# Kernel tuning notes

Hardware: AMD Instinct MI355X
Metric: run time of the kernel (lower is better)

Reference implementation:

```python
import jax, jax.numpy as jnp
import numpy as np

N = 4096
IN_F = 512
OUT_F = 64
HEADS = 4
ALPHA = 0.2  # leaky relu slope
NEG_INF = -9e15


def setup_inputs() -> dict:
    key = jax.random.key(0)
    k1, k2, k3, k4 = jax.random.split(key, 4)
    x = jax.random.normal(k1, (N, IN_F), dtype=jnp.float32)
    adj = jax.random.randint(k2, (N, N), 0, 2, dtype=jnp.int32)
    # xavier-uniform-like init for params
    limW = float(np.sqrt(6.0 / (IN_F + OUT_F * HEADS)))
    W = jax.random.uniform(k3, (IN_F, OUT_F * HEADS), dtype=jnp.float32, minval=-limW, maxval=limW)
    lima = float(np.sqrt(6.0 / (2 * OUT_F + 1)))
    a = jax.random.uniform(k4, (2 * OUT_F, 1), dtype=jnp.float32, minval=-lima, maxval=lima)
    return {"x": x, "adj": adj, "W": W, "a": a}


def reference(x, adj, W, a):
    # h: [N, H, F]
    h = (x @ W).reshape(N, HEADS, OUT_F)
    a_src = a[:OUT_F, 0]   # [F]
    a_dst = a[OUT_F:, 0]   # [F]
    s = jnp.einsum("nhf,f->nh", h, a_src)  # source-node score [N, H]
    t = jnp.einsum("nhf,f->nh", h, a_dst)  # dest-node score   [N, H]
    # e[i, j, k] = leaky_relu(s[i,k] + t[j,k]) -> [N, N, H]
    e = jax.nn.leaky_relu(s[:, None, :] + t[None, :, :], negative_slope=ALPHA)
    mask = (adj > 0)[:, :, None]  # [N, N, 1]
    e = jnp.where(mask, e, NEG_INF)
    attn = jax.nn.softmax(e, axis=1)  # softmax over neighbors j
    # weighted aggregation per head: [N, H, F]
    h_prime = jnp.einsum("ijh,jhf->ihf", attn, h)
    return h_prime.reshape(N, HEADS * OUT_F)
```

## Files before the change

kernel.cpp:

```cpp
#include <hip/hip_runtime.h>
#include <hip/hip_bf16.h>


#define NN 4096
#define KF 512
#define NF 256

typedef __attribute__((ext_vector_type(8))) short bf16x8;
typedef __attribute__((ext_vector_type(4))) short s16x4;
typedef __attribute__((ext_vector_type(4))) float f32x4;

union AB8 { bf16x8 v; short2 h[4]; short s[8]; int4 i4; };
union ST4 { s16x4 v; short2 h[2]; };
union I64 { long v; int i[2]; };

__device__ __forceinline__ short f2bf(float f) {
    union { float f; unsigned u; } v; v.f = f;
    unsigned r = v.u + 0x7fffu + ((v.u >> 16) & 1u);
    return (short)(r >> 16);
}
__device__ __forceinline__ short2 pkbf(float a, float b) {
    __hip_bfloat162 t = __float22bfloat162_rn(make_float2(a, b));
    union { __hip_bfloat162 v; short2 s; } u; u.v = t;
    return u.s;
}
__device__ __forceinline__ int pkfp8x4(float a, float b, float c, float d) {
    int p = __builtin_amdgcn_cvt_pk_fp8_f32(a, b, 0, false);
    p     = __builtin_amdgcn_cvt_pk_fp8_f32(c, d, p, true);
    return p;
}

__global__ __launch_bounds__(256) void xpack(const float* __restrict__ x,
                                             short* __restrict__ xF) {
    const int lane = threadIdx.x & 63, wv = threadIdx.x >> 6;
    const int i = blockIdx.x * 4 + wv;
    const float4* xp = (const float4*)(x + (size_t)i * KF + lane * 8);
    float4 xa = xp[0], xb = xp[1];
    ST4 o0, o1;
    o0.h[0] = pkbf(xa.x, xa.y); o0.h[1] = pkbf(xa.z, xa.w);
    o1.h[0] = pkbf(xb.x, xb.y); o1.h[1] = pkbf(xb.z, xb.w);
    const int kblk = lane >> 2, qk = lane & 3;
    const int jgrp = i >> 4, r = i & 15;
    short* dst = xF + ((size_t)(kblk * 256 + jgrp) * 64 + qk * 16 + r) * 8;
    *(s16x4*)dst = o0.v;
    *(s16x4*)(dst + 4) = o1.v;
}

__global__ __launch_bounds__(256) void wpack(const float* __restrict__ W,
                                             short* __restrict__ WtF) {
    int tid = blockIdx.x * 256 + threadIdx.x;
    int l = tid & 63, nt = (tid >> 6) & 3, hd = (tid >> 8) & 3, kblk = tid >> 10;
    int q = l >> 4, r = l & 15;
    int col = hd * 64 + nt * 16 + r;
    int k0 = kblk * 32 + q * 8;
    AB8 o;
    #pragma unroll
    for (int e = 0; e < 8; e++) o.s[e] = f2bf(W[(k0 + e) * NF + col]);
    *(bf16x8*)(WtF + (size_t)tid * 8) = o.v;
}

__global__ __launch_bounds__(256) void adjpack(const int* __restrict__ adj,
                                               unsigned* __restrict__ pT) {
    int gw   = (blockIdx.x * 256 + threadIdx.x) >> 6;
    int lane = threadIdx.x & 63;
    int i = gw >> 4, seg = gw & 15;
    const int* ap = adj + (size_t)i * NN + seg * 256 + lane;
    unsigned long long b0 = __ballot(ap[0]   != 0);
    unsigned long long b1 = __ballot(ap[64]  != 0);
    unsigned long long b2 = __ballot(ap[128] != 0);
    unsigned long long b3 = __ballot(ap[192] != 0);
    if (lane == 0) {
        *(uint4*)(pT + ((size_t)(seg * 2    ) * NN + i) * 4) =
            make_uint4((unsigned)b0, (unsigned)(b0 >> 32), (unsigned)b1, (unsigned)(b1 >> 32));
        *(uint4*)(pT + ((size_t)(seg * 2 + 1) * NN + i) * 4) =
            make_uint4((unsigned)b2, (unsigned)(b2 >> 32), (unsigned)b3, (unsigned)(b3 >> 32));
    }
}

__global__ __launch_bounds__(256) void gemmfuse(const short* __restrict__ xF,
                                                const short* __restrict__ WtF,
                                                const float* __restrict__ a,
                                                unsigned char* __restrict__ VtF8,
                                                float* __restrict__ ipk,
                                                float2* __restrict__ jpk) {
    const int lane = threadIdx.x & 63, wv = threadIdx.x >> 6;
    const int q = lane >> 4, r = lane & 15;
    const int jb32 = blockIdx.x >> 1, ch = blockIdx.x & 1;
    const int rg = wv >> 1, hd = ch * 2 + (wv & 1);
    const int jgrp = jb32 * 2 + rg;

    const short* ap = xF  + ((size_t)jgrp * 64 + lane) * 8;
    const short* wp = WtF + ((size_t)(hd * 4) * 64 + lane) * 8;

    f32x4 acc[4] = {};
    #pragma unroll
    for (int kblk = 0; kblk < 16; kblk++) {
        bf16x8 av = *(const bf16x8*)(ap + (size_t)kblk * 256 * 512);
        const short* w = wp + (size_t)kblk * 16 * 512;
        #pragma unroll
        for (int nt = 0; nt < 4; nt++) {
            bf16x8 bv = *(const bf16x8*)(w + nt * 512);
            acc[nt] = __builtin_amdgcn_mfma_f32_16x16x32_bf16(av, bv, acc[nt], 0, 0, 0);
        }
    }

    const int base = rg * 16 + q * 4;
    const int qa = base >> 3, e0 = base & 7;
    #pragma unroll
    for (int nt = 0; nt < 4; nt++) {
        size_t slot = (size_t)(((jb32 * 4 + hd) * 4 + nt) * 64 + qa * 16 + r);
        *(int*)(VtF8 + slot * 8 + e0) = pkfp8x4(acc[nt][0], acc[nt][1], acc[nt][2], acc[nt][3]);
    }

    float as[4], at[4];
    #pragma unroll
    for (int nt = 0; nt < 4; nt++) { as[nt] = a[nt * 16 + r]; at[nt] = a[64 + nt * 16 + r]; }
    f32x4 sp = {}, tp = {};
    #pragma unroll
    for (int nt = 0; nt < 4; nt++)
        #pragma unroll
        for (int reg = 0; reg < 4; reg++) {
            sp[reg] += acc[nt][reg] * as[nt];
            tp[reg] += acc[nt][reg] * at[nt];
        }
    #pragma unroll
    for (int d = 1; d < 16; d <<= 1)
        #pragma unroll
        for (int reg = 0; reg < 4; reg++) {
            sp[reg] += __shfl_xor(sp[reg], d, 64);
            tp[reg] += __shfl_xor(tp[reg], d, 64);
        }
    if (r == 0) {
        #pragma unroll
        for (int reg = 0; reg < 4; reg++) {
            int j = jb32 * 32 + rg * 16 + q * 4 + reg;
            ipk[hd * NN + j] = __expf(-0.8f * sp[reg]);
            jpk[hd * NN + j] = make_float2(__expf(tp[reg]), __expf(0.2f * tp[reg]));
        }
    }
}

struct PF { float4 ja, jb, jc, jd; long v0, v1, v2, v3; };

__global__ __launch_bounds__(1024) __attribute__((amdgpu_waves_per_eu(1, 4)))
void gat_attn(const uint4* __restrict__ pT4, const float* __restrict__ ipk,
              const float* __restrict__ jpkf, const unsigned char* __restrict__ VtF8,
              float* __restrict__ out) {
    const int tid = threadIdx.x, lane = tid & 63, wv = tid >> 6;
    const int hd = wv & 3, jq = wv >> 2;
    const int q = lane >> 4, r = lane & 15;
    const int i0 = blockIdx.x * 16, i = i0 + r;
    const float ci = ipk[hd * NN + i];
    const int qs = q * 8;
    const float* jpf = jpkf + (size_t)hd * NN * 2;

    f32x4 acc[5] = {};
    const long ones = 0x3838383838383838L;

    auto load_pf = [&](PF& p, int it) {
        const float4* jp = (const float4*)(jpf + 2 * ((jq << 10) + (it << 5) + qs));
        p.ja = jp[0]; p.jb = jp[1]; p.jc = jp[2]; p.jd = jp[3];
        const long* vp = (const long*)(VtF8 + (size_t)(((jq * 32 + it) * 16 + hd * 4) * 512) + lane * 8);
        p.v0 = vp[0]; p.v1 = vp[64]; p.v2 = vp[128]; p.v3 = vp[192];
    };
    auto consume = [&](const PF& p, unsigned w) {
        float p0 = (w & 1u)   ? fmaxf(p.ja.x, ci * p.ja.y) : 0.f;
        float p1 = (w & 2u)   ? fmaxf(p.ja.z, ci * p.ja.w) : 0.f;
        float p2 = (w & 4u)   ? fmaxf(p.jb.x, ci * p.jb.y) : 0.f;
        float p3 = (w & 8u)   ? fmaxf(p.jb.z, ci * p.jb.w) : 0.f;
        float p4 = (w & 16u)  ? fmaxf(p.jc.x, ci * p.jc.y) : 0.f;
        float p5 = (w & 32u)  ? fmaxf(p.jc.z, ci * p.jc.w) : 0.f;
        float p6 = (w & 64u)  ? fmaxf(p.jd.x, ci * p.jd.y) : 0.f;
        float p7 = (w & 128u) ? fmaxf(p.jd.z, ci * p.jd.w) : 0.f;
        I64 af;
        af.i[0] = pkfp8x4(p0, p1, p2, p3);
        af.i[1] = pkfp8x4(p4, p5, p6, p7);
        acc[0] = __builtin_amdgcn_mfma_f32_16x16x32_fp8_fp8(af.v, p.v0, acc[0], 0, 0, 0);
        acc[1] = __builtin_amdgcn_mfma_f32_16x16x32_fp8_fp8(af.v, p.v1, acc[1], 0, 0, 0);
        acc[2] = __builtin_amdgcn_mfma_f32_16x16x32_fp8_fp8(af.v, p.v2, acc[2], 0, 0, 0);
        acc[3] = __builtin_amdgcn_mfma_f32_16x16x32_fp8_fp8(af.v, p.v3, acc[3], 0, 0, 0);
        acc[4] = __builtin_amdgcn_mfma_f32_16x16x32_fp8_fp8(af.v, ones, acc[4], 0, 0, 0);
    };

    const uint4* prow = pT4 + (size_t)(jq * 8) * NN + i;
    uint4 wg = prow[0];
    PF pa, pb;
    load_pf(pa, 0);
    #pragma unroll 1
    for (int g = 0; g < 8; g++) {
        uint4 wgn = wg;
        if (g < 7) wgn = prow[(size_t)(g + 1) * NN];
        const int it = g * 4;
        load_pf(pb, it + 1); consume(pa, wg.x >> qs);
        load_pf(pa, it + 2); consume(pb, wg.y >> qs);
        load_pf(pb, it + 3); consume(pa, wg.z >> qs);
        if (g < 7) load_pf(pa, it + 4);
        consume(pb, wg.w >> qs);
        wg = wgn;
    }

    __shared__ float sacc[3][4][5][64][4];
    if (jq > 0) {
        const int gg = jq - 1;
        #pragma unroll
        for (int t = 0; t < 5; t++)
            *(f32x4*)&sacc[gg][hd][t][lane][0] = acc[t];
    }
    __syncthreads();
    if (jq == 0) {
        #pragma unroll
        for (int gg = 0; gg < 3; gg++)
            #pragma unroll
            for (int t = 0; t < 5; t++) {
                f32x4 o = *(const f32x4*)&sacc[gg][hd][t][lane][0];
                acc[t][0] += o[0]; acc[t][1] += o[1];
                acc[t][2] += o[2]; acc[t][3] += o[3];
            }
        #pragma unroll
        for (int reg = 0; reg < 4; reg++) {
            float inv = 1.f / acc[4][reg];
            int row = i0 + q * 4 + reg;
            #pragma unroll
            for (int t = 0; t < 4; t++)
                out[(size_t)row * NF + hd * 64 + t * 16 + r] = acc[t][reg] * inv;
        }
    }
}

extern "C" void kernel_launch(void* const* d_in, const int* in_sizes, int n_in,
                              void* d_out, int out_size, void* d_ws, size_t ws_size,
                              hipStream_t stream) {
    const float* x   = (const float*)d_in[0];
    const int*   adj = (const int*)d_in[1];
    const float* W   = (const float*)d_in[2];
    const float* a   = (const float*)d_in[3];
    float* out = (float*)d_out;

    char* ws = (char*)d_ws;
    short*         xF   = (short*)ws;
    short*         WtF  = (short*)(ws + 4194304);
    unsigned char* VtF8 = (unsigned char*)(ws + 4456448);
    unsigned*      pT   = (unsigned*)(ws + 5505024);
    float*         ipk  = (float*)(ws + 7602176);
    float2*        jpk  = (float2*)(ws + 7667712);

    xpack   <<<1024, 256, 0, stream>>>(x, xF);
    wpack   <<<64, 256, 0, stream>>>(W, WtF);
    adjpack <<<16384, 256, 0, stream>>>(adj, pT);
    gemmfuse<<<256, 256, 0, stream>>>(xF, WtF, a, VtF8, ipk, jpk);
    gat_attn<<<256, 1024, 0, stream>>>((const uint4*)pT, ipk, (const float*)jpk, VtF8, out);
}
```

Baseline: 150.1 us.

## Merge pack kernels into two launches and split attention grid per head

Combines xpack and wpack into one launch, and gemmfuse and adjpack into another, cutting five kernel launches to three so independent work overlaps. The attention kernel now uses one head per block with 8 waves splitting the neighbor range (1024 blocks of 512 threads instead of 256 of 1024), with a simpler non-prefetched load loop and an 8-way LDS reduction. This is meant to raise occupancy and reduce launch gaps, at the cost of losing explicit software prefetch and adding a longer serial reduction.

```diff
diff --git a/kernel.cpp b/kernel.cpp
--- a/kernel.cpp
+++ b/kernel.cpp
@@ -30,189 +30,180 @@
     return p;
 }
 
-__global__ __launch_bounds__(256) void xpack(const float* __restrict__ x,
-                                             short* __restrict__ xF) {
-    const int lane = threadIdx.x & 63, wv = threadIdx.x >> 6;
-    const int i = blockIdx.x * 4 + wv;
-    const float4* xp = (const float4*)(x + (size_t)i * KF + lane * 8);
-    float4 xa = xp[0], xb = xp[1];
-    ST4 o0, o1;
-    o0.h[0] = pkbf(xa.x, xa.y); o0.h[1] = pkbf(xa.z, xa.w);
-    o1.h[0] = pkbf(xb.x, xb.y); o1.h[1] = pkbf(xb.z, xb.w);
-    const int kblk = lane >> 2, qk = lane & 3;
-    const int jgrp = i >> 4, r = i & 15;
-    short* dst = xF + ((size_t)(kblk * 256 + jgrp) * 64 + qk * 16 + r) * 8;
-    *(s16x4*)dst = o0.v;
-    *(s16x4*)(dst + 4) = o1.v;
-}
-
-__global__ __launch_bounds__(256) void wpack(const float* __restrict__ W,
-                                             short* __restrict__ WtF) {
-    int tid = blockIdx.x * 256 + threadIdx.x;
-    int l = tid & 63, nt = (tid >> 6) & 3, hd = (tid >> 8) & 3, kblk = tid >> 10;
-    int q = l >> 4, r = l & 15;
-    int col = hd * 64 + nt * 16 + r;
-    int k0 = kblk * 32 + q * 8;
-    AB8 o;
-    #pragma unroll
-    for (int e = 0; e < 8; e++) o.s[e] = f2bf(W[(k0 + e) * NF + col]);
-    *(bf16x8*)(WtF + (size_t)tid * 8) = o.v;
-}
-
-__global__ __launch_bounds__(256) void adjpack(const int* __restrict__ adj,
-                                               unsigned* __restrict__ pT) {
-    int gw   = (blockIdx.x * 256 + threadIdx.x) >> 6;
-    int lane = threadIdx.x & 63;
-    int i = gw >> 4, seg = gw & 15;
-    const int* ap = adj + (size_t)i * NN + seg * 256 + lane;
-    unsigned long long b0 = __ballot(ap[0]   != 0);
-    unsigned long long b1 = __ballot(ap[64]  != 0);
-    unsigned long long b2 = __ballot(ap[128] != 0);
-    unsigned long long b3 = __ballot(ap[192] != 0);
-    if (lane == 0) {
-        *(uint4*)(pT + ((size_t)(seg * 2    ) * NN + i) * 4) =
-            make_uint4((unsigned)b0, (unsigned)(b0 >> 32), (unsigned)b1, (unsigned)(b1 >> 32));
-        *(uint4*)(pT + ((size_t)(seg * 2 + 1) * NN + i) * 4) =
-            make_uint4((unsigned)b2, (unsigned)(b2 >> 32), (unsigned)b3, (unsigned)(b3 >> 32));
-    }
-}
-
-__global__ __launch_bounds__(256) void gemmfuse(const short* __restrict__ xF,
-                                                const short* __restrict__ WtF,
-                                                const float* __restrict__ a,
-                                                unsigned char* __restrict__ VtF8,
-                                                float* __restrict__ ipk,
-                                                float2* __restrict__ jpk) {
-    const int lane = threadIdx.x & 63, wv = threadIdx.x >> 6;
-    const int q = lane >> 4, r = lane & 15;
-    const int jb32 = blockIdx.x >> 1, ch = blockIdx.x & 1;
-    const int rg = wv >> 1, hd = ch * 2 + (wv & 1);
-    const int jgrp = jb32 * 2 + rg;
-
-    const short* ap = xF  + ((size_t)jgrp * 64 + lane) * 8;
-    const short* wp = WtF + ((size_t)(hd * 4) * 64 + lane) * 8;
-
-    f32x4 acc[4] = {};
-    #pragma unroll
-    for (int kblk = 0; kblk < 16; kblk++) {
-        bf16x8 av = *(const bf16x8*)(ap + (size_t)kblk * 256 * 512);
-        const short* w = wp + (size_t)kblk * 16 * 512;
+__global__ __launch_bounds__(256) void stage1(const float* __restrict__ x,
+                                              const float* __restrict__ W,
+                                              short* __restrict__ xF,
+                                              short* __restrict__ WtF) {
+    if (blockIdx.x < 1024) {
+        const int lane = threadIdx.x & 63, wv = threadIdx.x >> 6;
+        const int i = blockIdx.x * 4 + wv;
+        const float4* xp = (const float4*)(x + (size_t)i * KF + lane * 8);
+        float4 xa = xp[0], xb = xp[1];
+        ST4 o0, o1;
+        o0.h[0] = pkbf(xa.x, xa.y); o0.h[1] = pkbf(xa.z, xa.w);
+        o1.h[0] = pkbf(xb.x, xb.y); o1.h[1] = pkbf(xb.z, xb.w);
+        const int kblk = lane >> 2, qk = lane & 3;
+        const int jgrp = i >> 4, r = i & 15;
+        short* dst = xF + ((size_t)(kblk * 256 + jgrp) * 64 + qk * 16 + r) * 8;
+        *(s16x4*)dst = o0.v;
+        *(s16x4*)(dst + 4) = o1.v;
+    } else {
+        int tid = (blockIdx.x - 1024) * 256 + threadIdx.x;
+        int l = tid & 63, nt = (tid >> 6) & 3, hd = (tid >> 8) & 3, kblk = tid >> 10;
+        int q = l >> 4, r = l & 15;
+        int col = hd * 64 + nt * 16 + r;
+        int k0 = kblk * 32 + q * 8;
+        AB8 o;
+        #pragma unroll
+        for (int e = 0; e < 8; e++) o.s[e] = f2bf(W[(k0 + e) * NF + col]);
+        *(bf16x8*)(WtF + (size_t)tid * 8) = o.v;
+    }
+}
+
+__global__ __launch_bounds__(256) void stage2(const short* __restrict__ xF,
+                                              const short* __restrict__ WtF,
+                                              const float* __restrict__ a,
+                                              const int* __restrict__ adj,
+                                              unsigned char* __restrict__ VtF8,
+                                              float* __restrict__ ipk,
+                                              float2* __restrict__ jpk,
+                                              unsigned* __restrict__ pT) {
+    if (blockIdx.x < 256) {
+        const int lane = threadIdx.x & 63, wv = threadIdx.x >> 6;
+        const int q = lane >> 4, r = lane & 15;
+        const int jb32 = blockIdx.x >> 1, ch = blockIdx.x & 1;
+        const int rg = wv >> 1, hd = ch * 2 + (wv & 1);
+        const int jgrp = jb32 * 2 + rg;
+
+        const short* ap = xF  + ((size_t)jgrp * 64 + lane) * 8;
+        const short* wp = WtF + ((size_t)(hd * 4) * 64 + lane) * 8;
+
+        f32x4 acc[4] = {};
+        #pragma unroll
+        for (int kblk = 0; kblk < 16; kblk++) {
+            bf16x8 av = *(const bf16x8*)(ap + (size_t)kblk * 256 * 512);
+            const short* w = wp + (size_t)kblk * 16 * 512;
+            #pragma unroll
+            for (int nt = 0; nt < 4; nt++) {
+                bf16x8 bv = *(const bf16x8*)(w + nt * 512);
+                acc[nt] = __builtin_amdgcn_mfma_f32_16x16x32_bf16(av, bv, acc[nt], 0, 0, 0);
+            }
+        }
+        const int base = rg * 16 + q * 4;
+        const int qa = base >> 3, e0 = base & 7;
         #pragma unroll
         for (int nt = 0; nt < 4; nt++) {
-            bf16x8 bv = *(const bf16x8*)(w + nt * 512);
-            acc[nt] = __builtin_amdgcn_mfma_f32_16x16x32_bf16(av, bv, acc[nt], 0, 0, 0);
-        }
-    }
-
-    const int base = rg * 16 + q * 4;
-    const int qa = base >> 3, e0 = base & 7;
-    #pragma unroll
-    for (int nt = 0; nt < 4; nt++) {
-        size_t slot = (size_t)(((jb32 * 4 + hd) * 4 + nt) * 64 + qa * 16 + r);
-        *(int*)(VtF8 + slot * 8 + e0) = pkfp8x4(acc[nt][0], acc[nt][1], acc[nt][2], acc[nt][3]);
-    }
-
-    float as[4], at[4];
-    #pragma unroll
-    for (int nt = 0; nt < 4; nt++) { as[nt] = a[nt * 16 + r]; at[nt] = a[64 + nt * 16 + r]; }
-    f32x4 sp = {}, tp = {};
-    #pragma unroll
-    for (int nt = 0; nt < 4; nt++)
-        #pragma unroll
-        for (int reg = 0; reg < 4; reg++) {
-            sp[reg] += acc[nt][reg] * as[nt];
-            tp[reg] += acc[nt][reg] * at[nt];
-        }
-    #pragma unroll
-    for (int d = 1; d < 16; d <<= 1)
-        #pragma unroll
-        for (int reg = 0; reg < 4; reg++) {
-            sp[reg] += __shfl_xor(sp[reg], d, 64);
-            tp[reg] += __shfl_xor(tp[reg], d, 64);
-        }
-    if (r == 0) {
-        #pragma unroll
-        for (int reg = 0; reg < 4; reg++) {
-            int j = jb32 * 32 + rg * 16 + q * 4 + reg;
-            ipk[hd * NN + j] = __expf(-0.8f * sp[reg]);
-            jpk[hd * NN + j] = make_float2(__expf(tp[reg]), __expf(0.2f * tp[reg]));
-        }
-    }
-}
-
-struct PF { float4 ja, jb, jc, jd; long v0, v1, v2, v3; };
-
-__global__ __launch_bounds__(1024) __attribute__((amdgpu_waves_per_eu(1, 4)))
+            size_t slot = (size_t)(((jb32 * 4 + hd) * 4 + nt) * 64 + qa * 16 + r);
+            *(int*)(VtF8 + slot * 8 + e0) = pkfp8x4(acc[nt][0], acc[nt][1], acc[nt][2], acc[nt][3]);
+        }
+        float as[4], at[4];
+        #pragma unroll
+        for (int nt = 0; nt < 4; nt++) { as[nt] = a[nt * 16 + r]; at[nt] = a[64 + nt * 16 + r]; }
+        f32x4 sp = {}, tp = {};
+        #pragma unroll
+        for (int nt = 0; nt < 4; nt++)
+            #pragma unroll
+            for (int reg = 0; reg < 4; reg++) {
+                sp[reg] += acc[nt][reg] * as[nt];
+                tp[reg] += acc[nt][reg] * at[nt];
+            }
+        #pragma unroll
+        for (int d = 1; d < 16; d <<= 1)
+            #pragma unroll
+            for (int reg = 0; reg < 4; reg++) {
+                sp[reg] += __shfl_xor(sp[reg], d, 64);
+                tp[reg] += __shfl_xor(tp[reg], d, 64);
+            }
+        if (r == 0) {
+            #pragma unroll
+            for (int reg = 0; reg < 4; reg++) {
+                int j = jb32 * 32 + rg * 16 + q * 4 + reg;
+                ipk[hd * NN + j] = __expf(-0.8f * sp[reg]);
+                jpk[hd * NN + j] = make_float2(__expf(tp[reg]), __expf(0.2f * tp[reg]));
+            }
+        }
+    } else {
+        int gw   = ((blockIdx.x - 256) * 256 + threadIdx.x) >> 6;
+        int lane = threadIdx.x & 63;
+        int i = gw >> 4, seg = gw & 15;
+        const int* ap = adj + (size_t)i * NN + seg * 256 + lane;
+        unsigned long long b0 = __ballot(ap[0]   != 0);
+        unsigned long long b1 = __ballot(ap[64]  != 0);
+        unsigned long long b2 = __ballot(ap[128] != 0);
+        unsigned long long b3 = __ballot(ap[192] != 0);
+        if (lane == 0) {
+            *(uint4*)(pT + ((size_t)(seg * 2    ) * NN + i) * 4) =
+                make_uint4((unsigned)b0, (unsigned)(b0 >> 32), (unsigned)b1, (unsigned)(b1 >> 32));
+            *(uint4*)(pT + ((size_t)(seg * 2 + 1) * NN + i) * 4) =
+                make_uint4((unsigned)b2, (unsigned)(b2 >> 32), (unsigned)b3, (unsigned)(b3 >> 32));
+        }
+    }
+}
+
+__global__ __launch_bounds__(512, 8)
 void gat_attn(const uint4* __restrict__ pT4, const float* __restrict__ ipk,
               const float* __restrict__ jpkf, const unsigned char* __restrict__ VtF8,
               float* __restrict__ out) {
-    const int tid = threadIdx.x, lane = tid & 63, wv = tid >> 6;
-    const int hd = wv & 3, jq = wv >> 2;
+    const int lane = threadIdx.x & 63, js = threadIdx.x >> 6;
+    const int hd = blockIdx.x & 3, itile = blockIdx.x >> 2;
     const int q = lane >> 4, r = lane & 15;
-    const int i0 = blockIdx.x * 16, i = i0 + r;
+    const int i0 = itile * 16, i = i0 + r;
     const float ci = ipk[hd * NN + i];
     const int qs = q * 8;
-    const float* jpf = jpkf + (size_t)hd * NN * 2;
 
     f32x4 acc[5] = {};
     const long ones = 0x3838383838383838L;
 
-    auto load_pf = [&](PF& p, int it) {
-        const float4* jp = (const float4*)(jpf + 2 * ((jq << 10) + (it << 5) + qs));
-        p.ja = jp[0]; p.jb = jp[1]; p.jc = jp[2]; p.jd = jp[3];
-        const long* vp = (const long*)(VtF8 + (size_t)(((jq * 32 + it) * 16 + hd * 4) * 512) + lane * 8);
-        p.v0 = vp[0]; p.v1 = vp[64]; p.v2 = vp[128]; p.v3 = vp[192];
-    };
-    auto consume = [&](const PF& p, unsigned w) {
-        float p0 = (w & 1u)   ? fmaxf(p.ja.x, ci * p.ja.y) : 0.f;
-        float p1 = (w & 2u)   ? fmaxf(p.ja.z, ci * p.ja.w) : 0.f;
-        float p2 = (w & 4u)   ? fmaxf(p.jb.x, ci * p.jb.y) : 0.f;
-        float p3 = (w & 8u)   ? fmaxf(p.jb.z, ci * p.jb.w) : 0.f;
-        float p4 = (w & 16u)  ? fmaxf(p.jc.x, ci * p.jc.y) : 0.f;
-        float p5 = (w & 32u)  ? fmaxf(p.jc.z, ci * p.jc.w) : 0.f;
-        float p6 = (w & 64u)  ? fmaxf(p.jd.x, ci * p.jd.y) : 0.f;
-        float p7 = (w & 128u) ? fmaxf(p.jd.z, ci * p.jd.w) : 0.f;
+    const int it0 = js * 16;
+    const float* jp = jpkf + (size_t)hd * NN * 2 + 2 * ((it0 << 5) + qs);
+    const long*  vp = (const long*)(VtF8 + (size_t)(it0 * 16 + hd * 4) * 512) + lane;
+    const uint4* prow = pT4 + (size_t)(js * 4) * NN + i;
+
+    auto consume = [&](unsigned w, float4 ja, float4 jb, float4 jc, float4 jd,
+                       long v0, long v1, long v2, long v3) {
+        float p0 = (w & 1u)   ? fmaxf(ja.x, ci * ja.y) : 0.f;
+        float p1 = (w & 2u)   ? fmaxf(ja.z, ci * ja.w) : 0.f;
+        float p2 = (w & 4u)   ? fmaxf(jb.x, ci * jb.y) : 0.f;
+        float p3 = (w & 8u)   ? fmaxf(jb.z, ci * jb.w) : 0.f;
+        float p4 = (w & 16u)  ? fmaxf(jc.x, ci * jc.y) : 0.f;
+        float p5 = (w & 32u)  ? fmaxf(jc.z, ci * jc.w) : 0.f;
+        float p6 = (w & 64u)  ? fmaxf(jd.x, ci * jd.y) : 0.f;
+        float p7 = (w & 128u) ? fmaxf(jd.z, ci * jd.w) : 0.f;
         I64 af;
         af.i[0] = pkfp8x4(p0, p1, p2, p3);
         af.i[1] = pkfp8x4(p4, p5, p6, p7);
-        acc[0] = __builtin_amdgcn_mfma_f32_16x16x32_fp8_fp8(af.v, p.v0, acc[0], 0, 0, 0);
-        acc[1] = __builtin_amdgcn_mfma_f32_16x16x32_fp8_fp8(af.v, p.v1, acc[1], 0, 0, 0);
-        acc[2] = __builtin_amdgcn_mfma_f32_16x16x32_fp8_fp8(af.v, p.v2, acc[2], 0, 0, 0);
-        acc[3] = __builtin_amdgcn_mfma_f32_16x16x32_fp8_fp8(af.v, p.v3, acc[3], 0, 0, 0);
+        acc[0] = __builtin_amdgcn_mfma_f32_16x16x32_fp8_fp8(af.v, v0, acc[0], 0, 0, 0);
+        acc[1] = __builtin_amdgcn_mfma_f32_16x16x32_fp8_fp8(af.v, v1, acc[1], 0, 0, 0);
+        acc[2] = __builtin_amdgcn_mfma_f32_16x16x32_fp8_fp8(af.v, v2, acc[2], 0, 0, 0);
+        acc[3] = __builtin_amdgcn_mfma_f32_16x16x32_fp8_fp8(af.v, v3, acc[3], 0, 0, 0);
         acc[4] = __builtin_amdgcn_mfma_f32_16x16x32_fp8_fp8(af.v, ones, acc[4], 0, 0, 0);
     };
 
-    const uint4* prow = pT4 + (size_t)(jq * 8) * NN + i;
-    uint4 wg = prow[0];
-    PF pa, pb;
-    load_pf(pa, 0);
     #pragma unroll 1
-    for (int g = 0; g < 8; g++) {
-        uint4 wgn = wg;
-        if (g < 7) wgn = prow[(size_t)(g + 1) * NN];
-        const int it = g * 4;
-        load_pf(pb, it + 1); consume(pa, wg.x >> qs);
-        load_pf(pa, it + 2); consume(pb, wg.y >> qs);
-        load_pf(pb, it + 3); consume(pa, wg.z >> qs);
-        if (g < 7) load_pf(pa, it + 4);
-        consume(pb, wg.w >> qs);
-        wg = wgn;
-    }
-
-    __shared__ float sacc[3][4][5][64][4];
-    if (jq > 0) {
-        const int gg = jq - 1;
+    for (int g = 0; g < 4; g++) {
+        uint4 wg = prow[(size_t)g * NN];
+        #pragma unroll
+        for (int u = 0; u < 4; u++) {
+            unsigned w = (u == 0 ? wg.x : u == 1 ? wg.y : u == 2 ? wg.z : wg.w) >> qs;
+            const float4* jpv = (const float4*)jp;
+            consume(w, jpv[0], jpv[1], jpv[2], jpv[3], vp[0], vp[64], vp[128], vp[192]);
+            jp += 64; vp += 1024;
+        }
+    }
+
+    __shared__ float sacc[7][5][64][4];
+    if (js > 0) {
         #pragma unroll
         for (int t = 0; t < 5; t++)
-            *(f32x4*)&sacc[gg][hd][t][lane][0] = acc[t];
+            *(f32x4*)&sacc[js - 1][t][lane][0] = acc[t];
     }
     __syncthreads();
-    if (jq == 0) {
-        #pragma unroll
-        for (int gg = 0; gg < 3; gg++)
+    if (js == 0) {
+        #pragma unroll 1
+        for (int gg = 0; gg < 7; gg++)
             #pragma unroll
             for (int t = 0; t < 5; t++) {
-                f32x4 o = *(const f32x4*)&sacc[gg][hd][t][lane][0];
+                f32x4 o = *(const f32x4*)&sacc[gg][t][lane][0];
                 acc[t][0] += o[0]; acc[t][1] += o[1];
                 acc[t][2] += o[2]; acc[t][3] += o[3];
             }
@@ -244,9 +235,7 @@
     float*         ipk  = (float*)(ws + 7602176);
     float2*        jpk  = (float2*)(ws + 7667712);
 
-    xpack   <<<1024, 256, 0, stream>>>(x, xF);
-    wpack   <<<64, 256, 0, stream>>>(W, WtF);
-    adjpack <<<16384, 256, 0, stream>>>(adj, pT);
-    gemmfuse<<<256, 256, 0, stream>>>(xF, WtF, a, VtF8, ipk, jpk);
-    gat_attn<<<256, 1024, 0, stream>>>((const uint4*)pT, ipk, (const float*)jpk, VtF8, out);
-}
+    stage1  <<<1088, 256, 0, stream>>>(x, W, xF, WtF);
+    stage2  <<<16640, 256, 0, stream>>>(xF, WtF, a, adj, VtF8, ipk, jpk, pT);
+    gat_attn<<<1024, 512, 0, stream>>>((const uint4*)pT, ipk, (const float*)jpk, VtF8, out);
+}
```

After: 141.7 us. 1.06x faster.
